# Performance work log

Measured on AMD Instinct MI355X. Metric: run time of the kernel, lower is better.

Reference implementation:

```python
import jax, jax.numpy as jnp
import numpy as np

N = 50000          # nodes
E = 400000         # edges
MUL = 32           # multiplicity per irrep
NUM_NEIGHBORS = 8.0
INV_SQRT3 = 1.0 / np.sqrt(3.0)  # w3j(1,1,0) coefficient


def setup_inputs() -> dict:
    key = jax.random.key(0)
    ks = jax.random.split(key, 20)
    inp = {
        # node_input: 32x0e (dim 32) + 32x1o (dim 96) = 128
        "node_input": jax.random.normal(ks[0], (N, 4 * MUL), jnp.float32),
        "node_attr": jnp.ones((N, 1), jnp.float32),           # 1x0e trivial attr
        "edge_src": jax.random.randint(ks[1], (E,), 0, N, jnp.int32),
        "edge_dst": jax.random.randint(ks[2], (E,), 0, N, jnp.int32),
        "edge_attr": jax.random.normal(ks[3], (E, 4), jnp.float32),   # 1x0e + 1x1o
        "edge_scalars": jax.random.normal(ks[4], (E, 16), jnp.float32),
        # FullyConnectedTensorProduct weights (uvw, node_attr has mul 1)
        "w_sc0": jax.random.normal(ks[5], (MUL, MUL), jnp.float32),
        "w_sc1": jax.random.normal(ks[6], (MUL, MUL), jnp.float32),
        "w_lin1_0": jax.random.normal(ks[7], (MUL, MUL), jnp.float32),
        "w_lin1_1": jax.random.normal(ks[8], (MUL, MUL), jnp.float32),
        # radial FC net -> per-edge TP weights (numel = 4*MUL = 128)
        "fc_w1": jax.random.normal(ks[9], (16, 64), jnp.float32),
        "fc_w2": jax.random.normal(ks[10], (64, 4 * MUL), jnp.float32),
        # lin2: irreps_mid (64x0e+64x1o) x attr -> output
        "w_lin2_0": jax.random.normal(ks[11], (2 * MUL, MUL), jnp.float32),
        "w_lin2_1": jax.random.normal(ks[12], (2 * MUL, MUL), jnp.float32),
        # alpha: irreps_mid x attr -> 0e (zero-init in original; small randn for a nontrivial test)
        "w_alpha": 0.1 * jax.random.normal(ks[13], (2 * MUL, 1), jnp.float32),
        # sc_edges: irreps_mid x edge_attr -> edge_attr
        "w_se0a": jax.random.normal(ks[14], (2 * MUL,), jnp.float32),  # mid0e x ea0e -> 0e
        "w_se0b": jax.random.normal(ks[15], (2 * MUL,), jnp.float32),  # mid1o x ea1o -> 0e
        "w_se1a": jax.random.normal(ks[16], (2 * MUL,), jnp.float32),  # mid0e x ea1o -> 1o
        "w_se1b": jax.random.normal(ks[17], (2 * MUL,), jnp.float32),  # mid1o x ea0e -> 1o
    }
    return inp


def reference(node_input, node_attr, edge_src, edge_dst, edge_attr, edge_scalars,
              w_sc0, w_sc1, w_lin1_0, w_lin1_1, fc_w1, fc_w2,
              w_lin2_0, w_lin2_1, w_alpha, w_se0a, w_se0b, w_se1a, w_se1b):
    inv_nn = 1.0 / jnp.sqrt(jnp.asarray(NUM_NEIGHBORS, node_input.dtype))
    n = node_input.shape[0]
    x0 = node_input[:, :MUL]                       # (N, 32)   32x0e
    x1 = node_input[:, MUL:].reshape(n, MUL, 3)    # (N, 32, 3) 32x1o
    a = node_attr                                  # (N, 1)
    s_in = 1.0 / np.sqrt(MUL)                      # FCTP fan-in normalization

    # self-connection: FCTP(input, attr) -> output
    sc0 = (x0 @ w_sc0) * a * s_in
    sc1 = jnp.einsum('num,uw->nwm', x1, w_sc1) * a[:, :, None] * s_in
    node_self = jnp.concatenate([sc0, sc1.reshape(n, 3 * MUL)], axis=1)  # (N, 128)

    # lin1: FCTP(input, attr) -> input irreps
    f0 = (x0 @ w_lin1_0) * a * s_in
    f1 = jnp.einsum('num,uw->nwm', x1, w_lin1_1) * a[:, :, None] * s_in

    # gather source node features per edge
    g0 = f0[edge_src]                              # (E, 32)
    g1 = f1[edge_src]                              # (E, 32, 3)
    ea0 = edge_attr[:, :1]                         # (E, 1)   1x0e
    ea1 = edge_attr[:, 1:]                         # (E, 3)   1x1o

    # radial net -> per-edge TP weights (FullyConnectedNet with sin activation)
    h = jnp.sin(edge_scalars @ fc_w1 * (1.0 / np.sqrt(16.0)))
    w = h @ fc_w2 * (1.0 / np.sqrt(64.0))          # (E, 128)
    wA, wB, wC, wD = jnp.split(w, 4, axis=1)       # each (E, 32)

    # uvu tensor product, 4 instructions
    mA = wA * g0 * ea0                                           # 0e x 0e -> 0e
    mD = wD * jnp.einsum('eum,em->eu', g1, ea1) * INV_SQRT3      # 1o x 1o -> 0e
    mB = (wB * g0)[:, :, None] * ea1[:, None, :]                 # 0e x 1o -> 1o
    mC = (wC[:, :, None] * g1) * ea0[:, :, None]                 # 1o x 0e -> 1o
    mid0 = jnp.concatenate([mA, mD], axis=1)       # (E, 64)  64x0e
    mid1 = jnp.concatenate([mB, mC], axis=1)       # (E, 64, 3) 64x1o

    # scatter-add to destination nodes
    n0 = jax.ops.segment_sum(mid0, edge_dst, num_segments=n) * inv_nn
    n1 = jax.ops.segment_sum(mid1, edge_dst, num_segments=n) * inv_nn

    s_mid = 1.0 / np.sqrt(2 * MUL)
    out0 = (n0 @ w_lin2_0) * a * s_mid
    out1 = jnp.einsum('num,uw->nwm', n1, w_lin2_1) * a[:, :, None] * s_mid
    node_conv = jnp.concatenate([out0, out1.reshape(n, 3 * MUL)], axis=1)

    # alpha gate (sc.output_mask is all ones here, so alpha = 1 - 1 + alpha*1)
    alpha = (n0 @ w_alpha) * a * s_mid             # (N, 1)
    node_conv_out = node_self + alpha * node_conv  # (N, 128)

    # sc_edges: FCTP(mid, edge_attr) -> edge_attr irreps; fan-in = 128 per output
    s_se = 1.0 / np.sqrt(4 * MUL)
    se0 = ((mid0 @ w_se0a) * ea0[:, 0]
           + jnp.einsum('eum,em,u->e', mid1, ea1, w_se0b) * INV_SQRT3) * s_se
    se1 = ((mid0 @ w_se1a)[:, None] * ea1
           + jnp.einsum('eum,u->em', mid1, w_se1b) * ea0) * s_se
    edge_conv_out = edge_attr + jnp.concatenate([se0[:, None], se1], axis=1) * inv_nn

    return node_conv_out, edge_conv_out
```

## Files before the change

### kernel.cpp

```cpp
#include <hip/hip_runtime.h>
#include <math.h>

#define N_NODES 50000
#define E_EDGES 400000
#define NPRE_BLOCKS 6250
#define NHIST_BLOCKS 1563
#define NEDGE_BLOCKS 6250

typedef _Float16 f16x2 __attribute__((ext_vector_type(2)));
typedef _Float16 f16x4 __attribute__((ext_vector_type(4)));
typedef _Float16 f16x8 __attribute__((ext_vector_type(8)));
typedef float    f32x4 __attribute__((ext_vector_type(4)));

static constexpr float S_IN      = 0.17677669529663687f;
static constexpr float S_MID     = 0.125f;
static constexpr float S_SE      = 0.08838834764831843f;
static constexpr float INV_NN    = 0.35355339059327373f;
static constexpr float INV_SQRT3 = 0.5773502691896258f;
static constexpr float FC1_S     = 0.25f;
static constexpr float FC2_S     = 0.125f;

#define BAR_LDS() asm volatile("s_waitcnt lgkmcnt(0)\n\ts_barrier" ::: "memory")

__device__ inline float wave_reduce_dpp(float v) {
    int x;
    x = __builtin_amdgcn_update_dpp(0, __float_as_int(v), 0x111, 0xf, 0xf, true); v += __int_as_float(x);
    x = __builtin_amdgcn_update_dpp(0, __float_as_int(v), 0x112, 0xf, 0xf, true); v += __int_as_float(x);
    x = __builtin_amdgcn_update_dpp(0, __float_as_int(v), 0x114, 0xf, 0xf, true); v += __int_as_float(x);
    x = __builtin_amdgcn_update_dpp(0, __float_as_int(v), 0x118, 0xf, 0xf, true); v += __int_as_float(x);
    x = __builtin_amdgcn_update_dpp(0, __float_as_int(v), 0x142, 0xa, 0xf, true); v += __int_as_float(x);
    x = __builtin_amdgcn_update_dpp(0, __float_as_int(v), 0x143, 0xc, 0xf, true); v += __int_as_float(x);
    return __int_as_float(__builtin_amdgcn_readlane(__float_as_int(v), 63));
}

__global__ __launch_bounds__(256) void pre_hist_kernel(
    const float* __restrict__ node_input, const float* __restrict__ node_attr,
    const float* __restrict__ w_sc0, const float* __restrict__ w_sc1,
    const float* __restrict__ w_lin1_0, const float* __restrict__ w_lin1_1,
    float* __restrict__ out_self, _Float16* __restrict__ ws_h,
    const int* __restrict__ edge_dst, int* __restrict__ counts,
    const float* __restrict__ edge_scalars, _Float16* __restrict__ ES_h,
    float* __restrict__ nacc)
{
    const int t = threadIdx.x;
    if (blockIdx.x >= NPRE_BLOCKS) {
        const int e = (blockIdx.x - NPRE_BLOCKS) * 256 + t;
        if (e < E_EDGES) {
            atomicAdd(&counts[edge_dst[e]], 1);
            const float4* s4 = (const float4*)edge_scalars + (size_t)e * 4;
            _Float16* dp = ES_h + (size_t)e * 16;
            #pragma unroll
            for (int i = 0; i < 4; ++i) {
                const float4 v = s4[i];
                f16x4 p = {(_Float16)v.x, (_Float16)v.y, (_Float16)v.z, (_Float16)v.w};
                *(f16x4*)&dp[i * 4] = p;
            }
        }
        return;
    }
    const int n0 = blockIdx.x * 8;
    __shared__ __align__(16) float sx[8 * 128];
    __shared__ float sa[8];
    ((float4*)sx)[t] = ((const float4*)(node_input + (size_t)n0 * 128))[t];
    {
        float4* nz = (float4*)(nacc + (size_t)n0 * 256);
        const float4 z4 = {0.f, 0.f, 0.f, 0.f};
        nz[t] = z4; nz[t + 256] = z4;
    }
    if (t < 8) sa[t] = node_attr[n0 + t];
    __syncthreads();

    const int half = t >> 7;
    const int idx  = t & 127;
    float wcol[32];
    int m = 0;
    if (idx < 32) {
        const float* __restrict__ W = half ? w_lin1_0 : w_sc0;
        #pragma unroll
        for (int u = 0; u < 32; ++u) wcol[u] = W[u * 32 + idx];
    } else {
        const float* __restrict__ W = half ? w_lin1_1 : w_sc1;
        const int j = idx - 32;
        const int w = j / 3; m = j % 3;
        #pragma unroll
        for (int u = 0; u < 32; ++u) wcol[u] = W[u * 32 + w];
    }
    #pragma unroll
    for (int k = 0; k < 8; ++k) {
        const float* x = sx + k * 128;
        float acc = 0.f;
        if (idx < 32) {
            #pragma unroll
            for (int u = 0; u < 32; ++u) acc += x[u] * wcol[u];
        } else {
            #pragma unroll
            for (int u = 0; u < 32; ++u) acc += x[32 + u * 3 + m] * wcol[u];
        }
        const float v = acc * sa[k] * S_IN;
        if (half) ws_h[(size_t)(n0 + k) * 128 + idx] = (_Float16)v;
        else      out_self[(size_t)(n0 + k) * 128 + idx] = v;
    }
}

__global__ __launch_bounds__(1024) void scan_block_kernel(
    const int* __restrict__ counts, int* __restrict__ cursor, int* __restrict__ bsum,
    const float* __restrict__ fc_w1, const float* __restrict__ fc_w2,
    const float* __restrict__ w_se0a, const float* __restrict__ w_se0b,
    const float* __restrict__ w_se1a, const float* __restrict__ w_se1b,
    _Float16* __restrict__ W2T_g, _Float16* __restrict__ W1T_g,
    _Float16* __restrict__ BT_g)
{
    const int t = threadIdx.x;
    if (blockIdx.x == 49) {
        for (int u = t; u < 8192; u += 1024) {
            const int k = u >> 7, c = u & 127;
            W2T_g[c * 72 + k] = (_Float16)fc_w2[u];
        }
        {
            W2T_g[(t >> 3) * 72 + 64 + (t & 7)] = (_Float16)0.f;
        }
        {
            const int j = t >> 4, k = t & 15;
            W1T_g[t] = (_Float16)fc_w1[k * 64 + j];
        }
        for (int u = t; u < 2112; u += 1024) BT_g[u] = (_Float16)0.f;
        __syncthreads();
        if (t < 256) {
            const int uu = t & 63, p = t >> 6;
            const float ev = (p == 0) ? w_se0a[uu] : w_se1b[uu];
            const float ov = (p == 0) ? w_se1a[uu] : w_se0b[uu];
            BT_g[(2 * p) * 264 + 4 * uu + p]     = (_Float16)ev;
            BT_g[(2 * p + 1) * 264 + 4 * uu + p] = (_Float16)ov;
        }
        return;
    }
    const int idx = blockIdx.x * 1024 + t;
    const int c   = (idx < N_NODES) ? counts[idx] : 0;
    int v = c, x;
    x = __builtin_amdgcn_update_dpp(0, v, 0x111, 0xf, 0xf, true); v += x;
    x = __builtin_amdgcn_update_dpp(0, v, 0x112, 0xf, 0xf, true); v += x;
    x = __builtin_amdgcn_update_dpp(0, v, 0x114, 0xf, 0xf, true); v += x;
    x = __builtin_amdgcn_update_dpp(0, v, 0x118, 0xf, 0xf, true); v += x;
    x = __builtin_amdgcn_update_dpp(0, v, 0x142, 0xa, 0xf, true); v += x;
    x = __builtin_amdgcn_update_dpp(0, v, 0x143, 0xc, 0xf, true); v += x;
    __shared__ int swv[16], sex[16];
    const int wid = t >> 6;
    if ((t & 63) == 63) swv[wid] = v;
    __syncthreads();
    if (t < 16) {
        int a = 0;
        for (int j = 0; j < t; ++j) a += swv[j];
        sex[t] = a;
        if (t == 15) bsum[blockIdx.x] = a + swv[15];
    }
    __syncthreads();
    if (idx < N_NODES) cursor[idx] = v - c + sex[wid];
}

__global__ __launch_bounds__(1024) void scan_fixup_kernel(
    int* __restrict__ cursor, const int* __restrict__ bsum)
{
    __shared__ int boff_s;
    const int t = threadIdx.x;
    if (t < 64) {
        int v = (t < (int)blockIdx.x) ? bsum[t] : 0;
        #pragma unroll
        for (int off = 32; off >= 1; off >>= 1) v += __shfl_down(v, off, 64);
        if (t == 0) boff_s = v;
    }
    __syncthreads();
    const int idx = blockIdx.x * 1024 + t;
    if (idx < N_NODES) cursor[idx] += boff_s;
}

__global__ __launch_bounds__(256) void scatter_kernel(
    const int* __restrict__ edge_dst, int* __restrict__ cursor,
    int* __restrict__ sorted_eid)
{
    const int e = blockIdx.x * 256 + threadIdx.x;
    if (e < E_EDGES) {
        const int p = atomicAdd(&cursor[edge_dst[e]], 1);
        sorted_eid[p] = e;
    }
}

__global__ __launch_bounds__(256, 5) void edge_kernel(
    const _Float16* __restrict__ ws_h,
    const int* __restrict__ edge_src, const int* __restrict__ edge_dst,
    const float* __restrict__ edge_attr, const _Float16* __restrict__ ES_h,
    const _Float16* __restrict__ W2T_g, const _Float16* __restrict__ W1T_g,
    const _Float16* __restrict__ BT_g,
    const int* __restrict__ sorted_eid,
    float* __restrict__ nacc, float* __restrict__ edge_out)
{
    __shared__ __align__(16) _Float16 sArena[15040];
    __shared__ __align__(16) float sEA[64 * 4];
    __shared__ __align__(16) float sDep[4][36];
    __shared__ int sSRC[64];
    __shared__ int sDST[64];
    __shared__ int sEID[64];

    _Float16* __restrict__ sW2T  = sArena;
    _Float16* __restrict__ sHT   = sArena + 9216;
    _Float16* __restrict__ sWt   = sArena;
    _Float16* __restrict__ sMidA = sArena + 8704;
    _Float16* __restrict__ sBT   = sArena + 12928;

    const int t    = threadIdx.x;
    const int lane = t & 63;
    const int wv   = t >> 6;
    const int quad = lane >> 4;
    const int mm   = lane & 15;

    const int orig = blockIdx.x;
    const int xcd  = orig & 7;
    constexpr int q = NEDGE_BLOCKS >> 3, r = NEDGE_BLOCKS & 7;
    const int bid = (xcd < r ? xcd * (q + 1) : r * (q + 1) + (xcd - r) * q) + (orig >> 3);
    const int e0 = bid * 64;
    const int eb = wv * 16;

    f16x8 a_w1[4];
    f16x8 b_es = {};
    if (quad < 2) {
        const int myeid = sorted_eid[e0 + eb + mm];
        b_es = *(const f16x8*)&ES_h[(size_t)myeid * 16 + quad * 8];
        #pragma unroll
        for (int jt = 0; jt < 4; ++jt)
            a_w1[jt] = *(const f16x8*)&W1T_g[(jt * 16 + mm) * 16 + quad * 8];
    } else {
        #pragma unroll
        for (int jt = 0; jt < 4; ++jt) a_w1[jt] = (f16x8){};
    }

    for (int i = t; i < 1152; i += 256)
        ((f16x8*)sW2T)[i] = ((const f16x8*)W2T_g)[i];
    if (t < 64) {
        const int eid = sorted_eid[e0 + t];
        *(float4*)&sEA[t * 4] = ((const float4*)edge_attr)[eid];
        sEID[t] = eid;
    } else if (t < 128) {
        sSRC[t - 64] = edge_src[sorted_eid[e0 + (t - 64)]];
    } else if (t < 192) {
        sDST[t - 128] = edge_dst[sorted_eid[e0 + (t - 128)]];
    }
    BAR_LDS();

    const bool hi = lane >= 32;
    const int  u  = lane - 32;
    const int idxA = hi ? (32 + 3 * u) : lane;
    const int idxB = hi ? (33 + 3 * u) : lane;
    const int idxC = hi ? (34 + 3 * u) : lane;
    const int col1 = hi ? (96 + u) : lane;
    const int col2 = hi ? (64 + u) : (32 + lane);

    float ga[4][4], gb[4][4], gc[4][4];
    #pragma unroll
    for (int i = 0; i < 4; ++i) {
        const _Float16* fr = ws_h + (size_t)sSRC[eb + i] * 128;
        ga[0][i] = (float)fr[idxA]; gb[0][i] = (float)fr[idxB]; gc[0][i] = (float)fr[idxC];
    }

    #pragma unroll
    for (int jt = 0; jt < 4; ++jt) {
        f32x4 d = {0.f, 0.f, 0.f, 0.f};
        d = __builtin_amdgcn_mfma_f32_16x16x32_f16(a_w1[jt], b_es, d, 0, 0, 0);
        f16x4 hv;
        hv[0] = (_Float16)__sinf(d[0] * FC1_S);
        hv[1] = (_Float16)__sinf(d[1] * FC1_S);
        hv[2] = (_Float16)__sinf(d[2] * FC1_S);
        hv[3] = (_Float16)__sinf(d[3] * FC1_S);
        *(f16x4*)&sHT[(eb + mm) * 72 + jt * 16 + quad * 4] = hv;
    }
    BAR_LDS();

    f32x4 dacc[8];
    {
        const f16x8 b_lo = *(const f16x8*)&sHT[(eb + mm) * 72 + quad * 8];
        const f16x8 b_hi = *(const f16x8*)&sHT[(eb + mm) * 72 + 32 + quad * 8];
        #pragma unroll
        for (int ct = 0; ct < 8; ++ct) {
            const f16x8 a_lo = *(const f16x8*)&sW2T[(ct * 16 + mm) * 72 + quad * 8];
            const f16x8 a_hi = *(const f16x8*)&sW2T[(ct * 16 + mm) * 72 + 32 + quad * 8];
            f32x4 d = {0.f, 0.f, 0.f, 0.f};
            d = __builtin_amdgcn_mfma_f32_16x16x32_f16(a_lo, b_lo, d, 0, 0, 0);
            d = __builtin_amdgcn_mfma_f32_16x16x32_f16(a_hi, b_hi, d, 0, 0, 0);
            dacc[ct] = d;
        }
    }
    BAR_LDS();

    {
        #pragma unroll
        for (int ct = 0; ct < 8; ++ct) {
            f16x4 v;
            v[0] = (_Float16)(dacc[ct][0] * FC2_S);
            v[1] = (_Float16)(dacc[ct][1] * FC2_S);
            v[2] = (_Float16)(dacc[ct][2] * FC2_S);
            v[3] = (_Float16)(dacc[ct][3] * FC2_S);
            *(f16x4*)&sWt[(eb + mm) * 136 + ct * 16 + quad * 4] = v;
        }
        for (int i = t; i < 264; i += 256)
            ((f16x8*)sBT)[i] = ((const f16x8*)BT_g)[i];
    }
    BAR_LDS();

    int   cur = -1;
    float am0 = 0.f, axx = 0.f, ayy = 0.f, azz = 0.f;
    _Float16* __restrict__ myA = sMidA + wv * 1056;
    const _Float16* __restrict__ arow = myA + (mm & 3) * 264;
    const _Float16* __restrict__ brow = sBT + (mm & 7) * 264;

    #pragma unroll
    for (int b = 0; b < 4; ++b) {
        if (b < 3) {
            #pragma unroll
            for (int i = 0; i < 4; ++i) {
                const _Float16* fr = ws_h + (size_t)sSRC[eb + (b + 1) * 4 + i] * 128;
                ga[b + 1][i] = (float)fr[idxA];
                gb[b + 1][i] = (float)fr[idxB];
                gc[b + 1][i] = (float)fr[idxC];
            }
        }
        #pragma unroll
        for (int i = 0; i < 4; ++i) {
            const int el  = eb + b * 4 + i;
            const int dst = sDST[el];
            const float ea0 = sEA[el * 4 + 0];
            const float e1x = sEA[el * 4 + 1];
            const float e1y = sEA[el * 4 + 2];
            const float e1z = sEA[el * 4 + 3];
            const float w1v = (float)sWt[el * 136 + col1];
            const float w2v = (float)sWt[el * 136 + col2];

            float mid0, m1x, m1y, m1z;
            if (!hi) {
                mid0 = w1v * ga[b][i] * ea0;
                const float wbg = w2v * ga[b][i];
                m1x = wbg * e1x; m1y = wbg * e1y; m1z = wbg * e1z;
            } else {
                const float dot = ga[b][i] * e1x + gb[b][i] * e1y + gc[b][i] * e1z;
                mid0 = w1v * dot * INV_SQRT3;
                const float wce = w2v * ea0;
                m1x = wce * ga[b][i]; m1y = wce * gb[b][i]; m1z = wce * gc[b][i];
            }

            if (dst != cur) {
                if (cur >= 0) {
                    float* np_ = nacc + (size_t)cur * 256;
                    atomicAdd(np_ + lane, am0);
                    atomicAdd(np_ + 64 + lane * 3 + 0, axx);
                    atomicAdd(np_ + 64 + lane * 3 + 1, ayy);
                    atomicAdd(np_ + 64 + lane * 3 + 2, azz);
                }
                cur = dst; am0 = axx = ayy = azz = 0.f;
            }
            am0 += mid0; axx += m1x; ayy += m1y; azz += m1z;

            f16x4 mv;
            mv[0] = (_Float16)mid0; mv[1] = (_Float16)m1x;
            mv[2] = (_Float16)m1y;  mv[3] = (_Float16)m1z;
            *(f16x4*)&myA[i * 264 + 4 * lane] = mv;
        }

        f32x4 d = {0.f, 0.f, 0.f, 0.f};
        #pragma unroll
        for (int ks = 0; ks < 8; ++ks) {
            const f16x8 a  = *(const f16x8*)&arow[ks * 32 + quad * 8];
            const f16x8 bb = *(const f16x8*)&brow[ks * 32 + quad * 8];
            d = __builtin_amdgcn_mfma_f32_16x16x32_f16(a, bb, d, 0, 0, 0);
        }
        if (lane < 8) {
            float4 f4; f4.x = d[0]; f4.y = d[1]; f4.z = d[2]; f4.w = d[3];
            *(float4*)&sDep[wv][lane * 4] = f4;
        }
        if (lane < 4) {
            const int el = eb + b * 4 + lane;
            const float c0 = sDep[wv][ 0 + lane], c1 = sDep[wv][ 4 + lane];
            const float c2 = sDep[wv][ 8 + lane], c3 = sDep[wv][12 + lane];
            const float c4 = sDep[wv][16 + lane], c5 = sDep[wv][20 + lane];
            const float c6 = sDep[wv][24 + lane], c7 = sDep[wv][28 + lane];
            const float ea0 = sEA[el * 4 + 0];
            const float e1x = sEA[el * 4 + 1];
            const float e1y = sEA[el * 4 + 2];
            const float e1z = sEA[el * 4 + 3];
            const float s0 = c0 * ea0 + (c3 * e1x + c5 * e1y + c7 * e1z) * INV_SQRT3;
            float4 o;
            o.x = ea0 + s0 * S_SE * INV_NN;
            o.y = e1x + (c1 * e1x + c2 * ea0) * S_SE * INV_NN;
            o.z = e1y + (c1 * e1y + c4 * ea0) * S_SE * INV_NN;
            o.w = e1z + (c1 * e1z + c6 * ea0) * S_SE * INV_NN;
            *(float4*)&edge_out[(size_t)sEID[el] * 4] = o;
        }
    }
    if (cur >= 0) {
        float* np_ = nacc + (size_t)cur * 256;
        atomicAdd(np_ + lane, am0);
        atomicAdd(np_ + 64 + lane * 3 + 0, axx);
        atomicAdd(np_ + 64 + lane * 3 + 1, ayy);
        atomicAdd(np_ + 64 + lane * 3 + 2, azz);
    }
}

__global__ __launch_bounds__(128) void node_post_kernel(
    const float* __restrict__ nacc, const float* __restrict__ node_attr,
    const float* __restrict__ w_lin2_0, const float* __restrict__ w_lin2_1,
    const float* __restrict__ w_alpha, float* __restrict__ out)
{
    const int n0 = blockIdx.x * 8, t = threadIdx.x;
    __shared__ __align__(16) float sn[8 * 256];
    __shared__ float salpha[8];
    const float4* src = (const float4*)(nacc + (size_t)n0 * 256);
    #pragma unroll
    for (int i = 0; i < 4; ++i) ((float4*)sn)[t + i * 128] = src[t + i * 128];
    __syncthreads();

    if (t < 64) {
        const float wa = w_alpha[t];
        #pragma unroll
        for (int k = 0; k < 8; ++k) {
            const float r = wave_reduce_dpp(sn[k * 256 + t] * wa);
            if (t == 0) salpha[k] = r;
        }
    }
    __syncthreads();

    float wcol[64];
    int m = 0;
    if (t < 32) {
        #pragma unroll
        for (int u = 0; u < 64; ++u) wcol[u] = w_lin2_0[u * 32 + t];
    } else {
        const int j = t - 32; const int w = j / 3; m = j % 3;
        #pragma unroll
        for (int u = 0; u < 64; ++u) wcol[u] = w_lin2_1[u * 32 + w];
    }
    #pragma unroll
    for (int k = 0; k < 8; ++k) {
        const float* s = sn + k * 256;
        float acc = 0.f;
        if (t < 32) {
            #pragma unroll
            for (int u = 0; u < 64; ++u) acc += s[u] * wcol[u];
        } else {
            #pragma unroll
            for (int u = 0; u < 64; ++u) acc += s[64 + u * 3 + m] * wcol[u];
        }
        const float a  = node_attr[n0 + k];
        const float sc = a * S_MID * INV_NN;
        const size_t o = (size_t)(n0 + k) * 128 + t;
        out[o] = out[o] + (salpha[k] * sc) * (acc * sc);
    }
}

extern "C" void kernel_launch(void* const* d_in, const int* in_sizes, int n_in,
                              void* d_out, int out_size, void* d_ws, size_t ws_size,
                              hipStream_t stream)
{
    const float* node_input   = (const float*)d_in[0];
    const float* node_attr    = (const float*)d_in[1];
    const int*   edge_src     = (const int*)d_in[2];
    const int*   edge_dst     = (const int*)d_in[3];
    const float* edge_attr    = (const float*)d_in[4];
    const float* edge_scalars = (const float*)d_in[5];
    const float* w_sc0        = (const float*)d_in[6];
    const float* w_sc1        = (const float*)d_in[7];
    const float* w_lin1_0     = (const float*)d_in[8];
    const float* w_lin1_1     = (const float*)d_in[9];
    const float* fc_w1        = (const float*)d_in[10];
    const float* fc_w2        = (const float*)d_in[11];
    const float* w_lin2_0     = (const float*)d_in[12];
    const float* w_lin2_1     = (const float*)d_in[13];
    const float* w_alpha      = (const float*)d_in[14];
    const float* w_se0a       = (const float*)d_in[15];
    const float* w_se0b       = (const float*)d_in[16];
    const float* w_se1a       = (const float*)d_in[17];
    const float* w_se1b       = (const float*)d_in[18];

    float* out      = (float*)d_out;
    float* edge_out = out + (size_t)N_NODES * 128;

    _Float16* ws_h = (_Float16*)d_ws;
    _Float16* ES_h = ws_h + (size_t)N_NODES * 128;
    float* nacc   = (float*)((char*)d_ws + (size_t)N_NODES * 128 * 4);
    int*   counts = (int*)(nacc + (size_t)N_NODES * 256);
    int*   cursor = counts + N_NODES;
    int*   sid    = cursor + N_NODES;
    int*   bsum   = sid + E_EDGES;
    _Float16* W2T_g = (_Float16*)(bsum + 64);
    _Float16* W1T_g = W2T_g + 9216;
    _Float16* BT_g  = W1T_g + 1024;

    hipMemsetAsync(counts, 0, N_NODES * sizeof(int), stream);

    pre_hist_kernel<<<NPRE_BLOCKS + NHIST_BLOCKS, 256, 0, stream>>>(
        node_input, node_attr, w_sc0, w_sc1, w_lin1_0, w_lin1_1, out, ws_h,
        edge_dst, counts, edge_scalars, ES_h, nacc);

    scan_block_kernel<<<50, 1024, 0, stream>>>(counts, cursor, bsum,
        fc_w1, fc_w2, w_se0a, w_se0b, w_se1a, w_se1b, W2T_g, W1T_g, BT_g);
    scan_fixup_kernel<<<49, 1024, 0, stream>>>(cursor, bsum);
    scatter_kernel<<<(E_EDGES + 255) / 256, 256, 0, stream>>>(edge_dst, cursor, sid);

    edge_kernel<<<NEDGE_BLOCKS, 256, 0, stream>>>(
        ws_h, edge_src, edge_dst, edge_attr, ES_h, W2T_g, W1T_g, BT_g,
        sid, nacc, edge_out);

    node_post_kernel<<<N_NODES / 8, 128, 0, stream>>>(
        nacc, node_attr, w_lin2_0, w_lin2_1, w_alpha, out);
}
```

Baseline: 416.8 us.

## Transpose vector irreps to component-major layout in LDS and node accumulator

Vector (1o) features are now stored component-major (m*mul + u) in shared memory and in the node accumulator. This lets the node pre/post matvecs read contiguous float4s and drop the divergent branch on the strided x[u*3+m] path. The edge kernel also issues all source-row gathers up front and caches the per-edge TP weights in registers before the scatter loop, trading higher register pressure for more memory-level parallelism. The accumulator layout change must stay consistent between the edge atomics and node_post.

```diff
diff --git a/kernel.cpp b/kernel.cpp
--- a/kernel.cpp
+++ b/kernel.cpp
@@ -61,7 +61,21 @@
     const int n0 = blockIdx.x * 8;
     __shared__ __align__(16) float sx[8 * 128];
     __shared__ float sa[8];
-    ((float4*)sx)[t] = ((const float4*)(node_input + (size_t)n0 * 128))[t];
+    {
+        const int k = t >> 5, q = t & 31;
+        const float4 v = ((const float4*)(node_input + (size_t)n0 * 128))[t];
+        if (q < 8) {
+            *(float4*)&sx[k * 128 + q * 4] = v;
+        } else {
+            const int base = q * 4 - 32;
+            const float vv[4] = {v.x, v.y, v.z, v.w};
+            #pragma unroll
+            for (int j = 0; j < 4; ++j) {
+                const int uj = (base + j) / 3, mj = (base + j) % 3;
+                sx[k * 128 + 32 + mj * 32 + uj] = vv[j];
+            }
+        }
+    }
     {
         float4* nz = (float4*)(nacc + (size_t)n0 * 256);
         const float4 z4 = {0.f, 0.f, 0.f, 0.f};
@@ -73,7 +87,7 @@
     const int half = t >> 7;
     const int idx  = t & 127;
     float wcol[32];
-    int m = 0;
+    int m = 0, xoff = 0;
     if (idx < 32) {
         const float* __restrict__ W = half ? w_lin1_0 : w_sc0;
         #pragma unroll
@@ -82,19 +96,21 @@
         const float* __restrict__ W = half ? w_lin1_1 : w_sc1;
         const int j = idx - 32;
         const int w = j / 3; m = j % 3;
+        xoff = 32 + m * 32;
         #pragma unroll
         for (int u = 0; u < 32; ++u) wcol[u] = W[u * 32 + w];
     }
     #pragma unroll
     for (int k = 0; k < 8; ++k) {
-        const float* x = sx + k * 128;
+        const float* xb = sx + k * 128 + xoff;
         float acc = 0.f;
-        if (idx < 32) {
-            #pragma unroll
-            for (int u = 0; u < 32; ++u) acc += x[u] * wcol[u];
-        } else {
-            #pragma unroll
-            for (int u = 0; u < 32; ++u) acc += x[32 + u * 3 + m] * wcol[u];
+        #pragma unroll
+        for (int u4 = 0; u4 < 8; ++u4) {
+            const f32x4 xv = *(const f32x4*)&xb[u4 * 4];
+            acc += xv[0] * wcol[u4 * 4 + 0];
+            acc += xv[1] * wcol[u4 * 4 + 1];
+            acc += xv[2] * wcol[u4 * 4 + 2];
+            acc += xv[3] * wcol[u4 * 4 + 3];
         }
         const float v = acc * sa[k] * S_IN;
         if (half) ws_h[(size_t)(n0 + k) * 128 + idx] = (_Float16)v;
@@ -255,10 +271,15 @@
 
     float ga[4][4], gb[4][4], gc[4][4];
     #pragma unroll
-    for (int i = 0; i < 4; ++i) {
-        const _Float16* fr = ws_h + (size_t)sSRC[eb + i] * 128;
-        ga[0][i] = (float)fr[idxA]; gb[0][i] = (float)fr[idxB]; gc[0][i] = (float)fr[idxC];
-    }
+    for (int b = 0; b < 4; ++b)
+        #pragma unroll
+        for (int i = 0; i < 4; ++i) {
+            const _Float16* fr = ws_h + (size_t)sSRC[eb + b * 4 + i] * 128;
+            ga[b][i] = (float)fr[idxA];
+            gb[b][i] = (float)fr[idxB];
+            gc[b][i] = (float)fr[idxC];
+        }
+    asm volatile("" ::: "memory");
 
     #pragma unroll
     for (int jt = 0; jt < 4; ++jt) {
@@ -304,6 +325,13 @@
     }
     BAR_LDS();
 
+    float w1f[16], w2f[16];
+    #pragma unroll
+    for (int e = 0; e < 16; ++e) {
+        w1f[e] = (float)sWt[(eb + e) * 136 + col1];
+        w2f[e] = (float)sWt[(eb + e) * 136 + col2];
+    }
+
     int   cur = -1;
     float am0 = 0.f, axx = 0.f, ayy = 0.f, azz = 0.f;
     _Float16* __restrict__ myA = sMidA + wv * 1056;
@@ -312,15 +340,6 @@
 
     #pragma unroll
     for (int b = 0; b < 4; ++b) {
-        if (b < 3) {
-            #pragma unroll
-            for (int i = 0; i < 4; ++i) {
-                const _Float16* fr = ws_h + (size_t)sSRC[eb + (b + 1) * 4 + i] * 128;
-                ga[b + 1][i] = (float)fr[idxA];
-                gb[b + 1][i] = (float)fr[idxB];
-                gc[b + 1][i] = (float)fr[idxC];
-            }
-        }
         #pragma unroll
         for (int i = 0; i < 4; ++i) {
             const int el  = eb + b * 4 + i;
@@ -329,8 +348,8 @@
             const float e1x = sEA[el * 4 + 1];
             const float e1y = sEA[el * 4 + 2];
             const float e1z = sEA[el * 4 + 3];
-            const float w1v = (float)sWt[el * 136 + col1];
-            const float w2v = (float)sWt[el * 136 + col2];
+            const float w1v = w1f[b * 4 + i];
+            const float w2v = w2f[b * 4 + i];
 
             float mid0, m1x, m1y, m1z;
             if (!hi) {
@@ -348,9 +367,9 @@
                 if (cur >= 0) {
                     float* np_ = nacc + (size_t)cur * 256;
                     atomicAdd(np_ + lane, am0);
-                    atomicAdd(np_ + 64 + lane * 3 + 0, axx);
-                    atomicAdd(np_ + 64 + lane * 3 + 1, ayy);
-                    atomicAdd(np_ + 64 + lane * 3 + 2, azz);
+                    atomicAdd(np_ + 64 + lane, axx);
+                    atomicAdd(np_ + 128 + lane, ayy);
+                    atomicAdd(np_ + 192 + lane, azz);
                 }
                 cur = dst; am0 = axx = ayy = azz = 0.f;
             }
@@ -395,9 +414,9 @@
     if (cur >= 0) {
         float* np_ = nacc + (size_t)cur * 256;
         atomicAdd(np_ + lane, am0);
-        atomicAdd(np_ + 64 + lane * 3 + 0, axx);
-        atomicAdd(np_ + 64 + lane * 3 + 1, ayy);
-        atomicAdd(np_ + 64 + lane * 3 + 2, azz);
+        atomicAdd(np_ + 64 + lane, axx);
+        atomicAdd(np_ + 128 + lane, ayy);
+        atomicAdd(np_ + 192 + lane, azz);
     }
 }
 
@@ -425,25 +444,27 @@
     __syncthreads();
 
     float wcol[64];
-    int m = 0;
+    int xoff = 0;
     if (t < 32) {
         #pragma unroll
         for (int u = 0; u < 64; ++u) wcol[u] = w_lin2_0[u * 32 + t];
     } else {
-        const int j = t - 32; const int w = j / 3; m = j % 3;
+        const int j = t - 32; const int w = j / 3; const int m = j % 3;
+        xoff = 64 + m * 64;
         #pragma unroll
         for (int u = 0; u < 64; ++u) wcol[u] = w_lin2_1[u * 32 + w];
     }
     #pragma unroll
     for (int k = 0; k < 8; ++k) {
-        const float* s = sn + k * 256;
+        const float* xb = sn + k * 256 + xoff;
         float acc = 0.f;
-        if (t < 32) {
-            #pragma unroll
-            for (int u = 0; u < 64; ++u) acc += s[u] * wcol[u];
-        } else {
-            #pragma unroll
-            for (int u = 0; u < 64; ++u) acc += s[64 + u * 3 + m] * wcol[u];
+        #pragma unroll
+        for (int u4 = 0; u4 < 16; ++u4) {
+            const f32x4 xv = *(const f32x4*)&xb[u4 * 4];
+            acc += xv[0] * wcol[u4 * 4 + 0];
+            acc += xv[1] * wcol[u4 * 4 + 1];
+            acc += xv[2] * wcol[u4 * 4 + 2];
+            acc += xv[3] * wcol[u4 * 4 + 3];
         }
         const float a  = node_attr[n0 + k];
         const float sc = a * S_MID * INV_NN;
```

Measured after the change: 386.7 us. 7.2% less time.
